# Optimization experiments

Hardware: AMD Instinct MI355X
Metric: run time of the kernel (lower is better)

The kernel has to match this reference:

```python
import jax, jax.numpy as jnp
import numpy as np

B, Q, H = 32, 1024, 1024
HR = H // 2          # reduced hidden size (reduction_factor=2)
C = 4096             # codebook size (num_tokens)
COMMIT_W = 0.25


def setup_inputs() -> dict:
    key = jax.random.key(0)
    ks = jax.random.split(key, 10)
    s = lambda fan: 1.0 / np.sqrt(fan)
    return {
        "x": jax.random.normal(ks[0], (B, Q, H), dtype=jnp.float32),
        # encoder: Linear(H,H) -> ReLU -> Linear(H,HR)
        "enc_w1": jax.random.normal(ks[1], (H, H), jnp.float32) * s(H),
        "enc_b1": jnp.zeros((H,), jnp.float32),
        "enc_w2": jax.random.normal(ks[2], (H, HR), jnp.float32) * s(H),
        "enc_b2": jnp.zeros((HR,), jnp.float32),
        # codebook: [C, HR]
        "codebook": jax.random.normal(ks[3], (C, HR), jnp.float32),
        # decoder: Linear(HR,H) -> ReLU -> Linear(H,H)
        "dec_w1": jax.random.normal(ks[4], (HR, H), jnp.float32) * s(HR),
        "dec_b1": jnp.zeros((H,), jnp.float32),
        "dec_w2": jax.random.normal(ks[5], (H, H), jnp.float32) * s(H),
        "dec_b2": jnp.zeros((H,), jnp.float32),
    }


def reference(x, enc_w1, enc_b1, enc_w2, enc_b2, codebook,
              dec_w1, dec_b1, dec_w2, dec_b2):
    # prepare_input = Identity (normalize=False)
    # encoder MLP
    h = jax.nn.relu(jnp.einsum("bqh,hk->bqk", x, enc_w1) + enc_b1)
    z = jnp.einsum("bqh,hr->bqr", h, enc_w2) + enc_b2          # [B,Q,HR] pre-quant

    # nearest-codebook search: argmin_c ||z - e_c||^2 (expand, skip z^2 term)
    zf = z.reshape(-1, HR)                                      # [N,HR]
    d = (jnp.sum(codebook * codebook, axis=-1)[None, :]
         - 2.0 * zf @ codebook.T)                               # [N,C]
    idx = jnp.argmin(d, axis=-1)                                # [N]
    quantized = codebook[idx].reshape(B, Q, HR)                 # gather lookup

    # straight-through estimator + commitment loss
    quantized_st = z + jax.lax.stop_gradient(quantized - z)
    commit_loss = COMMIT_W * jnp.mean(
        (z - jax.lax.stop_gradient(quantized)) ** 2)

    # decoder MLP
    h2 = jax.nn.relu(jnp.einsum("bqr,rh->bqh", quantized_st, dec_w1) + dec_b1)
    recon = jnp.einsum("bqh,hk->bqk", h2, dec_w2) + dec_b2      # [B,Q,H]

    token_indices = idx.reshape(B, Q)
    return recon, quantized_st, token_indices, commit_loss
```

## Files before the change

kernel.cpp:

```cpp
#include <hip/hip_runtime.h>


#define BM 128
#define BN 128
#define BK 16
#define TM 8
#define TN 8

#define NROW 32768
#define HDIM 1024
#define HRDIM 512
#define CODES 4096

typedef __attribute__((ext_vector_type(8))) short bf16x8;
typedef __attribute__((ext_vector_type(4))) float f32x4;

__global__ __launch_bounds__(256) void sgemm_bias(
    const float* __restrict__ A, const float* __restrict__ B,
    const float* __restrict__ bias, float* __restrict__ C,
    int M, int N, int K, int do_relu)
{
    __shared__ __align__(16) float As[BK][BM + 4];
    __shared__ __align__(16) float Bs[BK][BN + 4];

    const int tid = threadIdx.x;
    const int tx = tid & 15;
    const int ty = tid >> 4;
    const int block_row = blockIdx.y * BM;
    const int block_col = blockIdx.x * BN;

    float acc[TM][TN] = {};

    const int a_r0 = tid >> 2;
    const int a_c0 = (tid & 3) << 2;
    const int b_r0 = tid >> 5;
    const int b_c0 = (tid & 31) << 2;

    const float* Ab = A + (size_t)block_row * K;

    for (int k0 = 0; k0 < K; k0 += BK) {
#pragma unroll
        for (int i = 0; i < 2; ++i) {
            int r = a_r0 + i * 64;
            float4 v = *(const float4*)(Ab + (size_t)r * K + k0 + a_c0);
            As[a_c0 + 0][r] = v.x;
            As[a_c0 + 1][r] = v.y;
            As[a_c0 + 2][r] = v.z;
            As[a_c0 + 3][r] = v.w;
        }
#pragma unroll
        for (int i = 0; i < 2; ++i) {
            int r = b_r0 + i * 8;
            float4 v = *(const float4*)(B + (size_t)(k0 + r) * N + block_col + b_c0);
            *(float4*)(&Bs[r][b_c0]) = v;
        }
        __syncthreads();
#pragma unroll
        for (int k = 0; k < BK; ++k) {
            float4 a0 = *(const float4*)(&As[k][ty * 8]);
            float4 a1 = *(const float4*)(&As[k][ty * 8 + 4]);
            float4 b0 = *(const float4*)(&Bs[k][tx * 4]);
            float4 b1 = *(const float4*)(&Bs[k][tx * 4 + 64]);
            float am[TM] = {a0.x, a0.y, a0.z, a0.w, a1.x, a1.y, a1.z, a1.w};
            float bn[TN] = {b0.x, b0.y, b0.z, b0.w, b1.x, b1.y, b1.z, b1.w};
#pragma unroll
            for (int i = 0; i < TM; ++i)
#pragma unroll
                for (int j = 0; j < TN; ++j)
                    acc[i][j] = fmaf(am[i], bn[j], acc[i][j]);
        }
        __syncthreads();
    }

    float4 bv0 = *(const float4*)(bias + block_col + tx * 4);
    float4 bv1 = *(const float4*)(bias + block_col + 64 + tx * 4);
#pragma unroll
    for (int i = 0; i < TM; ++i) {
        int gr = block_row + ty * TM + i;
        float* Crow = C + (size_t)gr * N + block_col;
        float4 v0, v1;
        v0.x = acc[i][0] + bv0.x;  v0.y = acc[i][1] + bv0.y;
        v0.z = acc[i][2] + bv0.z;  v0.w = acc[i][3] + bv0.w;
        v1.x = acc[i][4] + bv1.x;  v1.y = acc[i][5] + bv1.y;
        v1.z = acc[i][6] + bv1.z;  v1.w = acc[i][7] + bv1.w;
        if (do_relu) {
            v0.x = fmaxf(v0.x, 0.0f); v0.y = fmaxf(v0.y, 0.0f);
            v0.z = fmaxf(v0.z, 0.0f); v0.w = fmaxf(v0.w, 0.0f);
            v1.x = fmaxf(v1.x, 0.0f); v1.y = fmaxf(v1.y, 0.0f);
            v1.z = fmaxf(v1.z, 0.0f); v1.w = fmaxf(v1.w, 0.0f);
        }
        *(float4*)(Crow + tx * 4) = v0;
        *(float4*)(Crow + 64 + tx * 4) = v1;
    }
}

__global__ __launch_bounds__(256) void cb2_kernel(const float* __restrict__ CB,
                                                  float* __restrict__ cb2,
                                                  unsigned int* __restrict__ cb2max)
{
    int row = blockIdx.x * 4 + (threadIdx.x >> 6);
    int lane = threadIdx.x & 63;
    const float* cr = CB + (size_t)row * HRDIM;
    float s = 0.0f;
#pragma unroll
    for (int i = 0; i < 2; ++i) {
        int c = lane * 4 + i * 256;
        float4 v = *(const float4*)(cr + c);
        s = fmaf(v.x, v.x, s);
        s = fmaf(v.y, v.y, s);
        s = fmaf(v.z, v.z, s);
        s = fmaf(v.w, v.w, s);
    }
#pragma unroll
    for (int off = 32; off > 0; off >>= 1) s += __shfl_down(s, off, 64);
    if (lane == 0) {
        cb2[row] = s;
        atomicMax(cb2max, __float_as_uint(s));
    }
}

__device__ __forceinline__ unsigned short f2bf(float f)
{
    unsigned int u = __float_as_uint(f);
    return (unsigned short)((u + 0x7FFFu + ((u >> 16) & 1u)) >> 16);
}

__global__ __launch_bounds__(256) void to_bf16(const float* __restrict__ in,
                                               unsigned short* __restrict__ out,
                                               int nvec)
{
    int i = blockIdx.x * 256 + threadIdx.x;
    if (i >= nvec) return;
    float4 a = ((const float4*)in)[2 * i];
    float4 b = ((const float4*)in)[2 * i + 1];
    ushort4 o0, o1;
    o0.x = f2bf(a.x); o0.y = f2bf(a.y); o0.z = f2bf(a.z); o0.w = f2bf(a.w);
    o1.x = f2bf(b.x); o1.y = f2bf(b.y); o1.z = f2bf(b.z); o1.w = f2bf(b.w);
    ((ushort4*)out)[2 * i] = o0;
    ((ushort4*)out)[2 * i + 1] = o1;
}

__global__ __launch_bounds__(256) void coarse_dist(
    const unsigned short* __restrict__ Zh, const unsigned short* __restrict__ CBh,
    const float* __restrict__ cb2, float* __restrict__ localmin)
{
    __shared__ __align__(16) unsigned short As[128 * 64];
    __shared__ __align__(16) unsigned short Bs[128 * 64];
    __shared__ __align__(16) float sm[128][4];

    const int tid = threadIdx.x;
    const int lane = tid & 63;
    const int w = tid >> 6;
    const int wr = w >> 1, wc = w & 1;
    const int block_row = blockIdx.y * 128;
    const int block_col = blockIdx.x * 128;

    f32x4 acc[4][4] = {};

    for (int k0 = 0; k0 < HRDIM; k0 += 64) {
#pragma unroll
        for (int i = 0; i < 4; ++i) {
            int e = (tid + i * 256) * 8;
            int r = e >> 6;
            int c = e & 63;
            int addr = (r * 128 + c * 2) ^ ((r & 7) << 4);
            uint4 va = *(const uint4*)(Zh + (size_t)(block_row + r) * HRDIM + k0 + c);
            *(uint4*)((char*)As + addr) = va;
            uint4 vb = *(const uint4*)(CBh + (size_t)(block_col + r) * HRDIM + k0 + c);
            *(uint4*)((char*)Bs + addr) = vb;
        }
        __syncthreads();
#pragma unroll
        for (int kk = 0; kk < 2; ++kk) {
            bf16x8 af[4], bfr[4];
#pragma unroll
            for (int m = 0; m < 4; ++m) {
                int R = wr * 64 + m * 16 + (lane & 15);
                int byte = (R * 128 + (kk * 32 + (lane >> 4) * 8) * 2) ^ ((R & 7) << 4);
                af[m] = *(const bf16x8*)((const char*)As + byte);
            }
#pragma unroll
            for (int n = 0; n < 4; ++n) {
                int R = wc * 64 + n * 16 + (lane & 15);
                int byte = (R * 128 + (kk * 32 + (lane >> 4) * 8) * 2) ^ ((R & 7) << 4);
                bfr[n] = *(const bf16x8*)((const char*)Bs + byte);
            }
#pragma unroll
            for (int m = 0; m < 4; ++m)
#pragma unroll
                for (int n = 0; n < 4; ++n)
                    acc[m][n] = __builtin_amdgcn_mfma_f32_16x16x32_bf16(
                        af[m], bfr[n], acc[m][n], 0, 0, 0);
        }
        __syncthreads();
    }

    float c2[4];
#pragma unroll
    for (int n = 0; n < 4; ++n)
        c2[n] = cb2[block_col + wc * 64 + n * 16 + (lane & 15)];

#pragma unroll
    for (int m = 0; m < 4; ++m) {
#pragma unroll
        for (int g = 0; g < 2; ++g) {
#pragma unroll
            for (int q = 0; q < 4; ++q) {
                float d0 = c2[g * 2 + 0] - 2.0f * acc[m][g * 2 + 0][q];
                float d1 = c2[g * 2 + 1] - 2.0f * acc[m][g * 2 + 1][q];
                float v = fminf(d0, d1);
#pragma unroll
                for (int msk = 1; msk < 16; msk <<= 1)
                    v = fminf(v, __shfl_xor(v, msk, 64));
                if ((lane & 15) == 0) {
                    int rl = wr * 64 + m * 16 + (lane >> 4) * 4 + q;
                    sm[rl][wc * 2 + g] = v;
                }
            }
        }
    }
    __syncthreads();
    if (tid < 128) {
        float4 v4 = *(const float4*)(&sm[tid][0]);
        *(float4*)(localmin + (size_t)(block_row + tid) * 128 + (block_col >> 5)) = v4;
    }
}

__device__ __forceinline__ unsigned int float_orderkey(float f)
{
    unsigned int u = __float_as_uint(f);
    return (u & 0x80000000u) ? ~u : (u | 0x80000000u);
}

__global__ __launch_bounds__(256) void recheck(
    const float* __restrict__ Z, const float* __restrict__ CB,
    const float* __restrict__ cb2, const float* __restrict__ localmin,
    const unsigned int* __restrict__ cb2max,
    unsigned long long* __restrict__ packed)
{
    __shared__ __align__(16) float zs[HRDIM];
    __shared__ float lm[128];
    __shared__ float red[8];
    __shared__ unsigned long long bred[4];

    const int row = blockIdx.x;
    const int tid = threadIdx.x;

    float2 zv = ((const float2*)(Z + (size_t)row * HRDIM))[tid];
    ((float2*)zs)[tid] = zv;
    float z2p = zv.x * zv.x + zv.y * zv.y;
#pragma unroll
    for (int off = 32; off > 0; off >>= 1) z2p += __shfl_down(z2p, off, 64);

    float lmv = 1e30f;
    if (tid < 128) {
        lmv = localmin[(size_t)row * 128 + tid];
        lm[tid] = lmv;
    }
#pragma unroll
    for (int off = 32; off > 0; off >>= 1)
        lmv = fminf(lmv, __shfl_down(lmv, off, 64));
    if ((tid & 63) == 0) {
        red[tid >> 6] = z2p;
        red[4 + (tid >> 6)] = lmv;
    }
    __syncthreads();
    const float z2 = red[0] + red[1] + red[2] + red[3];
    const float m = fminf(fminf(red[4], red[5]), fminf(red[6], red[7]));
    const float thr = m + 0.05f * sqrtf(z2 * __uint_as_float(*cb2max)) + 0.01f;

    const int col_in_g = tid >> 3;
    const int sub = tid & 7;
    unsigned long long best = 0xFFFFFFFFFFFFFFFFull;

    for (int g = 0; g < 128; ++g) {
        if (lm[g] <= thr) {
            int c = g * 32 + col_in_g;
            const float4* cbp = (const float4*)(CB + (size_t)c * HRDIM) + sub * 16;
            const float4* zp = (const float4*)zs + sub * 16;
            float dot = 0.0f;
#pragma unroll
            for (int j = 0; j < 16; ++j) {
                float4 cv = cbp[j];
                float4 zq = zp[j];
                dot = fmaf(cv.x, zq.x, dot);
                dot = fmaf(cv.y, zq.y, dot);
                dot = fmaf(cv.z, zq.z, dot);
                dot = fmaf(cv.w, zq.w, dot);
            }
#pragma unroll
            for (int off = 4; off > 0; off >>= 1) dot += __shfl_down(dot, off, 64);
            if (sub == 0) {
                float d = cb2[c] - 2.0f * dot;
                unsigned long long p =
                    ((unsigned long long)float_orderkey(d) << 32) | (unsigned int)c;
                best = (p < best) ? p : best;
            }
        }
    }
#pragma unroll
    for (int off = 32; off > 0; off >>= 1) {
        unsigned long long o = __shfl_down(best, off, 64);
        best = (o < best) ? o : best;
    }
    if ((tid & 63) == 0) bred[tid >> 6] = best;
    __syncthreads();
    if (tid == 0) {
        unsigned long long b = bred[0];
        b = (bred[1] < b) ? bred[1] : b;
        b = (bred[2] < b) ? bred[2] : b;
        b = (bred[3] < b) ? bred[3] : b;
        packed[row] = b;
    }
}

__global__ __launch_bounds__(256) void gather_pass(
    const float* __restrict__ Z, const unsigned long long* __restrict__ packed,
    const float* __restrict__ CB, float* __restrict__ Q,
    float* __restrict__ IDX, float* __restrict__ partials)
{
    __shared__ float s[4];
    int row = blockIdx.x * 4 + (threadIdx.x >> 6);
    int lane = threadIdx.x & 63;

    unsigned long long p = packed[row];
    int idx = (int)(unsigned int)(p & 0xFFFFFFFFull);

    const float* zr = Z + (size_t)row * HRDIM;
    const float* cr = CB + (size_t)idx * HRDIM;
    float* qr = Q + (size_t)row * HRDIM;

    float z2 = 0.0f;
#pragma unroll
    for (int i = 0; i < 2; ++i) {
        int c = lane * 4 + i * 256;
        float4 zv = *(const float4*)(zr + c);
        float4 cv = *(const float4*)(cr + c);
        *(float4*)(qr + c) = cv;
        z2 = fmaf(zv.x, zv.x, z2);
        z2 = fmaf(zv.y, zv.y, z2);
        z2 = fmaf(zv.z, zv.z, z2);
        z2 = fmaf(zv.w, zv.w, z2);
    }
#pragma unroll
    for (int off = 32; off > 0; off >>= 1) z2 += __shfl_down(z2, off, 64);

    if (lane == 0) {
        unsigned int u = (unsigned int)(p >> 32);
        unsigned int bits = (u & 0x80000000u) ? (u ^ 0x80000000u) : ~u;
        float dmin = __uint_as_float(bits);
        IDX[row] = (float)idx;
        s[threadIdx.x >> 6] = z2 + dmin;
    }
    __syncthreads();
    if (threadIdx.x == 0) partials[blockIdx.x] = s[0] + s[1] + s[2] + s[3];
}

__global__ __launch_bounds__(256) void commit_final(
    const float* __restrict__ partials, int n, float* __restrict__ outv)
{
    __shared__ float s[256];
    float v = 0.0f;
    for (int i = threadIdx.x; i < n; i += 256) v += partials[i];
    s[threadIdx.x] = v;
    __syncthreads();
    for (int st = 128; st > 0; st >>= 1) {
        if (threadIdx.x < st) s[threadIdx.x] += s[threadIdx.x + st];
        __syncthreads();
    }
    if (threadIdx.x == 0)
        outv[0] = 0.25f * s[0] / (float)(NROW * HRDIM);
}

extern "C" void kernel_launch(void* const* d_in, const int* in_sizes, int n_in,
                              void* d_out, int out_size, void* d_ws, size_t ws_size,
                              hipStream_t stream)
{
    const float* x   = (const float*)d_in[0];
    const float* ew1 = (const float*)d_in[1];
    const float* eb1 = (const float*)d_in[2];
    const float* ew2 = (const float*)d_in[3];
    const float* eb2 = (const float*)d_in[4];
    const float* cb  = (const float*)d_in[5];
    const float* dw1 = (const float*)d_in[6];
    const float* db1 = (const float*)d_in[7];
    const float* dw2 = (const float*)d_in[8];
    const float* db2 = (const float*)d_in[9];

    float* out   = (float*)d_out;
    float* recon = out;
    float* qst   = out + 33554432;
    float* idxf  = out + 33554432 + 16777216;
    float* loss  = out + 33554432 + 16777216 + 32768;

    char* ws = (char*)d_ws;
    float* h = (float*)ws;
    unsigned short* zh  = (unsigned short*)ws;
    unsigned short* cbh = (unsigned short*)(ws + (size_t)33554432);
    float* localmin = (float*)(ws + (size_t)37748736);
    unsigned long long* packed =
        (unsigned long long*)(ws + (size_t)134217728);
    float* cb2      = (float*)(ws + (size_t)134217728 + 262144);
    float* partials = (float*)(ws + (size_t)134217728 + 262144 + 16384);
    unsigned int* cb2max =
        (unsigned int*)(ws + (size_t)134217728 + 262144 + 16384 + 32768);
    float* z = recon;

    hipMemsetAsync(cb2max, 0, 4, stream);
    cb2_kernel<<<CODES / 4, 256, 0, stream>>>(cb, cb2, cb2max);

    sgemm_bias<<<dim3(HDIM / BN, NROW / BM), 256, 0, stream>>>(
        x, ew1, eb1, h, NROW, HDIM, HDIM, 1);
    sgemm_bias<<<dim3(HRDIM / BN, NROW / BM), 256, 0, stream>>>(
        h, ew2, eb2, z, NROW, HRDIM, HDIM, 0);

    to_bf16<<<(NROW * HRDIM / 8 + 255) / 256, 256, 0, stream>>>(
        z, zh, NROW * HRDIM / 8);
    to_bf16<<<(CODES * HRDIM / 8 + 255) / 256, 256, 0, stream>>>(
        cb, cbh, CODES * HRDIM / 8);
    coarse_dist<<<dim3(CODES / 128, NROW / 128), 256, 0, stream>>>(
        zh, cbh, cb2, localmin);
    recheck<<<NROW, 256, 0, stream>>>(z, cb, cb2, localmin, cb2max, packed);
    gather_pass<<<NROW / 4, 256, 0, stream>>>(z, packed, cb, qst, idxf, partials);

    sgemm_bias<<<dim3(HDIM / BN, NROW / BM), 256, 0, stream>>>(
        qst, dw1, db1, h, NROW, HDIM, HRDIM, 1);
    sgemm_bias<<<dim3(HDIM / BN, NROW / BM), 256, 0, stream>>>(
        h, dw2, db2, recon, NROW, HDIM, HDIM, 0);

    commit_final<<<1, 256, 0, stream>>>(partials, NROW / 4, loss);
}
```

Baseline: 4.001 ms.

## Fuse candidate recheck with codebook gather, one wave per row

Merges the exact-distance recheck and the gather/commit-partial kernels into one kernel. Each 64-lane wave now handles one row, using a ballot mask over the coarse local minima to visit only candidate groups, with two lanes per codeword, instead of one 256-thread block per row looping over all 128 groups. This removes a kernel launch, the packed-index round trip through memory and a second read of z, and drops block-level syncs from the search. In exchange each wave handles candidate groups one after another, so a row with many candidates keeps its wave busy for longer.

```diff
diff --git a/kernel.cpp b/kernel.cpp
--- a/kernel.cpp
+++ b/kernel.cpp
@@ -232,128 +232,105 @@
     return (u & 0x80000000u) ? ~u : (u | 0x80000000u);
 }
 
-__global__ __launch_bounds__(256) void recheck(
+__global__ __launch_bounds__(256) void recheck_gather(
     const float* __restrict__ Z, const float* __restrict__ CB,
     const float* __restrict__ cb2, const float* __restrict__ localmin,
     const unsigned int* __restrict__ cb2max,
-    unsigned long long* __restrict__ packed)
-{
-    __shared__ __align__(16) float zs[HRDIM];
-    __shared__ float lm[128];
-    __shared__ float red[8];
-    __shared__ unsigned long long bred[4];
-
-    const int row = blockIdx.x;
+    float* __restrict__ Q, float* __restrict__ IDX, float* __restrict__ partials)
+{
+    __shared__ __align__(16) float zs[4][HRDIM];
+    __shared__ float spart[4];
+
     const int tid = threadIdx.x;
-
-    float2 zv = ((const float2*)(Z + (size_t)row * HRDIM))[tid];
-    ((float2*)zs)[tid] = zv;
-    float z2p = zv.x * zv.x + zv.y * zv.y;
-#pragma unroll
-    for (int off = 32; off > 0; off >>= 1) z2p += __shfl_down(z2p, off, 64);
-
-    float lmv = 1e30f;
-    if (tid < 128) {
-        lmv = localmin[(size_t)row * 128 + tid];
-        lm[tid] = lmv;
-    }
-#pragma unroll
-    for (int off = 32; off > 0; off >>= 1)
-        lmv = fminf(lmv, __shfl_down(lmv, off, 64));
-    if ((tid & 63) == 0) {
-        red[tid >> 6] = z2p;
-        red[4 + (tid >> 6)] = lmv;
-    }
-    __syncthreads();
-    const float z2 = red[0] + red[1] + red[2] + red[3];
-    const float m = fminf(fminf(red[4], red[5]), fminf(red[6], red[7]));
+    const int wv = tid >> 6;
+    const int lane = tid & 63;
+    const int row = blockIdx.x * 4 + wv;
+
+    const float* zr = Z + (size_t)row * HRDIM;
+    float4 z0 = *(const float4*)(zr + lane * 4);
+    float4 z1 = *(const float4*)(zr + lane * 4 + 256);
+    *(float4*)(&zs[wv][lane * 4]) = z0;
+    *(float4*)(&zs[wv][lane * 4 + 256]) = z1;
+    float z2 = 0.0f;
+    z2 = fmaf(z0.x, z0.x, z2); z2 = fmaf(z0.y, z0.y, z2);
+    z2 = fmaf(z0.z, z0.z, z2); z2 = fmaf(z0.w, z0.w, z2);
+    z2 = fmaf(z1.x, z1.x, z2); z2 = fmaf(z1.y, z1.y, z2);
+    z2 = fmaf(z1.z, z1.z, z2); z2 = fmaf(z1.w, z1.w, z2);
+#pragma unroll
+    for (int off = 32; off > 0; off >>= 1) z2 += __shfl_xor(z2, off, 64);
+
+    float lm0 = localmin[(size_t)row * 128 + lane];
+    float lm1 = localmin[(size_t)row * 128 + 64 + lane];
+    float m = fminf(lm0, lm1);
+#pragma unroll
+    for (int off = 32; off > 0; off >>= 1) m = fminf(m, __shfl_xor(m, off, 64));
+
     const float thr = m + 0.05f * sqrtf(z2 * __uint_as_float(*cb2max)) + 0.01f;
 
-    const int col_in_g = tid >> 3;
-    const int sub = tid & 7;
+    unsigned long long mask0 = __ballot(lm0 <= thr);
+    unsigned long long mask1 = __ballot(lm1 <= thr);
+
+    const int colh = lane >> 1;
+    const int half = lane & 1;
+    const float* zbase = &zs[wv][half * 256];
+
     unsigned long long best = 0xFFFFFFFFFFFFFFFFull;
 
-    for (int g = 0; g < 128; ++g) {
-        if (lm[g] <= thr) {
-            int c = g * 32 + col_in_g;
-            const float4* cbp = (const float4*)(CB + (size_t)c * HRDIM) + sub * 16;
-            const float4* zp = (const float4*)zs + sub * 16;
-            float dot = 0.0f;
-#pragma unroll
-            for (int j = 0; j < 16; ++j) {
-                float4 cv = cbp[j];
-                float4 zq = zp[j];
-                dot = fmaf(cv.x, zq.x, dot);
-                dot = fmaf(cv.y, zq.y, dot);
-                dot = fmaf(cv.z, zq.z, dot);
-                dot = fmaf(cv.w, zq.w, dot);
-            }
-#pragma unroll
-            for (int off = 4; off > 0; off >>= 1) dot += __shfl_down(dot, off, 64);
-            if (sub == 0) {
-                float d = cb2[c] - 2.0f * dot;
-                unsigned long long p =
-                    ((unsigned long long)float_orderkey(d) << 32) | (unsigned int)c;
-                best = (p < best) ? p : best;
-            }
-        }
-    }
-#pragma unroll
-    for (int off = 32; off > 0; off >>= 1) {
-        unsigned long long o = __shfl_down(best, off, 64);
+    while (mask0 | mask1) {
+        int g;
+        if (mask0) {
+            g = __builtin_ctzll(mask0);
+            mask0 &= mask0 - 1;
+        } else {
+            g = 64 + __builtin_ctzll(mask1);
+            mask1 &= mask1 - 1;
+        }
+        const int col = g * 32 + colh;
+        const float4* cp = (const float4*)(CB + (size_t)col * HRDIM + half * 256);
+        const float4* zp = (const float4*)zbase;
+        float d0 = 0.0f, d1 = 0.0f, d2 = 0.0f, d3 = 0.0f;
+#pragma unroll 4
+        for (int j = 0; j < 64; j += 4) {
+            float4 c0 = cp[j + 0], c1 = cp[j + 1], c2v = cp[j + 2], c3 = cp[j + 3];
+            float4 q0 = zp[j + 0], q1 = zp[j + 1], q2 = zp[j + 2], q3 = zp[j + 3];
+            d0 = fmaf(c0.x, q0.x, d0); d0 = fmaf(c0.y, q0.y, d0);
+            d0 = fmaf(c0.z, q0.z, d0); d0 = fmaf(c0.w, q0.w, d0);
+            d1 = fmaf(c1.x, q1.x, d1); d1 = fmaf(c1.y, q1.y, d1);
+            d1 = fmaf(c1.z, q1.z, d1); d1 = fmaf(c1.w, q1.w, d1);
+            d2 = fmaf(c2v.x, q2.x, d2); d2 = fmaf(c2v.y, q2.y, d2);
+            d2 = fmaf(c2v.z, q2.z, d2); d2 = fmaf(c2v.w, q2.w, d2);
+            d3 = fmaf(c3.x, q3.x, d3); d3 = fmaf(c3.y, q3.y, d3);
+            d3 = fmaf(c3.z, q3.z, d3); d3 = fmaf(c3.w, q3.w, d3);
+        }
+        float dot = (d0 + d1) + (d2 + d3);
+        dot += __shfl_xor(dot, 1, 64);
+        float d = cb2[col] - 2.0f * dot;
+        unsigned long long p =
+            ((unsigned long long)float_orderkey(d) << 32) | (unsigned int)col;
+        best = (p < best) ? p : best;
+    }
+
+#pragma unroll
+    for (int msk = 1; msk < 64; msk <<= 1) {
+        unsigned long long o = __shfl_xor(best, msk, 64);
         best = (o < best) ? o : best;
     }
-    if ((tid & 63) == 0) bred[tid >> 6] = best;
-    __syncthreads();
-    if (tid == 0) {
-        unsigned long long b = bred[0];
-        b = (bred[1] < b) ? bred[1] : b;
-        b = (bred[2] < b) ? bred[2] : b;
-        b = (bred[3] < b) ? bred[3] : b;
-        packed[row] = b;
-    }
-}
-
-__global__ __launch_bounds__(256) void gather_pass(
-    const float* __restrict__ Z, const unsigned long long* __restrict__ packed,
-    const float* __restrict__ CB, float* __restrict__ Q,
-    float* __restrict__ IDX, float* __restrict__ partials)
-{
-    __shared__ float s[4];
-    int row = blockIdx.x * 4 + (threadIdx.x >> 6);
-    int lane = threadIdx.x & 63;
-
-    unsigned long long p = packed[row];
-    int idx = (int)(unsigned int)(p & 0xFFFFFFFFull);
-
-    const float* zr = Z + (size_t)row * HRDIM;
+
+    const int idx = (int)(unsigned int)(best & 0xFFFFFFFFull);
     const float* cr = CB + (size_t)idx * HRDIM;
     float* qr = Q + (size_t)row * HRDIM;
-
-    float z2 = 0.0f;
-#pragma unroll
-    for (int i = 0; i < 2; ++i) {
-        int c = lane * 4 + i * 256;
-        float4 zv = *(const float4*)(zr + c);
-        float4 cv = *(const float4*)(cr + c);
-        *(float4*)(qr + c) = cv;
-        z2 = fmaf(zv.x, zv.x, z2);
-        z2 = fmaf(zv.y, zv.y, z2);
-        z2 = fmaf(zv.z, zv.z, z2);
-        z2 = fmaf(zv.w, zv.w, z2);
-    }
-#pragma unroll
-    for (int off = 32; off > 0; off >>= 1) z2 += __shfl_down(z2, off, 64);
+    *(float4*)(qr + lane * 4) = *(const float4*)(cr + lane * 4);
+    *(float4*)(qr + lane * 4 + 256) = *(const float4*)(cr + lane * 4 + 256);
 
     if (lane == 0) {
-        unsigned int u = (unsigned int)(p >> 32);
+        unsigned int u = (unsigned int)(best >> 32);
         unsigned int bits = (u & 0x80000000u) ? (u ^ 0x80000000u) : ~u;
         float dmin = __uint_as_float(bits);
         IDX[row] = (float)idx;
-        s[threadIdx.x >> 6] = z2 + dmin;
+        spart[wv] = z2 + dmin;
     }
     __syncthreads();
-    if (threadIdx.x == 0) partials[blockIdx.x] = s[0] + s[1] + s[2] + s[3];
+    if (tid == 0) partials[blockIdx.x] = spart[0] + spart[1] + spart[2] + spart[3];
 }
 
 __global__ __launch_bounds__(256) void commit_final(
@@ -398,8 +375,6 @@
     unsigned short* zh  = (unsigned short*)ws;
     unsigned short* cbh = (unsigned short*)(ws + (size_t)33554432);
     float* localmin = (float*)(ws + (size_t)37748736);
-    unsigned long long* packed =
-        (unsigned long long*)(ws + (size_t)134217728);
     float* cb2      = (float*)(ws + (size_t)134217728 + 262144);
     float* partials = (float*)(ws + (size_t)134217728 + 262144 + 16384);
     unsigned int* cb2max =
@@ -420,8 +395,8 @@
         cb, cbh, CODES * HRDIM / 8);
     coarse_dist<<<dim3(CODES / 128, NROW / 128), 256, 0, stream>>>(
         zh, cbh, cb2, localmin);
-    recheck<<<NROW, 256, 0, stream>>>(z, cb, cb2, localmin, cb2max, packed);
-    gather_pass<<<NROW / 4, 256, 0, stream>>>(z, packed, cb, qst, idxf, partials);
+    recheck_gather<<<NROW / 4, 256, 0, stream>>>(
+        z, cb, cb2, localmin, cb2max, qst, idxf, partials);
 
     sgemm_bias<<<dim3(HDIM / BN, NROW / BM), 256, 0, stream>>>(
         qst, dw1, db1, h, NROW, HDIM, HRDIM, 1);
```

New measurement: 4.189 ms. +4.7%, slower.
